# Kernel optimization log

Hardware: AMD Instinct MI355X
Metric: run time of the kernel (lower is better)

Reference implementation:

```python
import jax, jax.numpy as jnp
import numpy as np

EMBED_DICT = 200
EMBED_DIM = 16
HIDDEN = 32
LSTM_DIM = 256
B, C, L = 8192, 16, 64
END_IDX = 1  # stand-in for token_list.index('<End>')


def _lin(k, i, o):
    return jax.random.normal(k, (i, o), jnp.float32) * (1.0 / np.sqrt(i))


def setup_inputs() -> dict:
    key = jax.random.key(0)
    ks = jax.random.split(key, 20)
    feat_in = EMBED_DIM * 14 + LSTM_DIM  # 480
    z = lambda n: jnp.zeros((n,), jnp.float32)
    return {
        "trees": jax.random.randint(ks[0], (B, 1 + C, 17), 0, L),
        "lstm_out_list": jax.random.normal(ks[1], (B, L, 1, LSTM_DIM), jnp.float32),
        "first_notes": jax.random.normal(ks[2], (B, EMBED_DIM), jnp.float32),
        "train": 1,
        "embedding": jax.random.normal(ks[3], (EMBED_DICT, EMBED_DIM), jnp.float32) * 0.05,
        "leaf_end_W": _lin(ks[4], EMBED_DIM, HIDDEN), "leaf_end_b": z(HIDDEN),
        "lc_W1": _lin(ks[5], feat_in, HIDDEN * 4), "lc_b1": z(HIDDEN * 4),
        "lc_W2": _lin(ks[6], HIDDEN * 4, HIDDEN), "lc_b2": z(HIDDEN),
        "cs_W1": _lin(ks[7], HIDDEN * 2, HIDDEN * 4), "cs_b1": z(HIDDEN * 4),
        "cs_W2": _lin(ks[8], HIDDEN * 4, HIDDEN), "cs_b2": z(HIDDEN),
        "nf_W1": _lin(ks[9], feat_in, HIDDEN * 4), "nf_b1": z(HIDDEN * 4),
        "nf_W2": _lin(ks[10], HIDDEN * 4, HIDDEN), "nf_b2": z(HIDDEN),
        "cb_W1": _lin(ks[11], HIDDEN * 2, HIDDEN * 4), "cb_b1": z(HIDDEN * 4),
        "cb_W2": _lin(ks[12], HIDDEN * 4, HIDDEN), "cb_b2": z(HIDDEN),
        "ff_W1": _lin(ks[13], HIDDEN, HIDDEN), "ff_b1": z(HIDDEN),
        "ff_W2": _lin(ks[14], HIDDEN, HIDDEN), "ff_b2": z(HIDDEN),
        "ts_W": _lin(ks[15], HIDDEN, 1), "ts_b": z(1),
    }


def _mlp2(x, W1, b1, W2, b2):
    # Linear -> ReLU -> Linear -> ReLU (matches nn.Sequential blocks)
    return jax.nn.relu(jax.nn.relu(x @ W1 + b1) @ W2 + b2)


def reference(trees, lstm_out_list, first_notes, train, embedding,
              leaf_end_W, leaf_end_b, lc_W1, lc_b1, lc_W2, lc_b2,
              cs_W1, cs_b1, cs_W2, cs_b2, nf_W1, nf_b1, nf_W2, nf_b2,
              cb_W1, cb_b1, cb_W2, cb_b2, ff_W1, ff_b1, ff_W2, ff_b2,
              ts_W, ts_b):
    Bn = trees.shape[0]
    root = trees[:, 0, :]        # (B, 17)
    leaves = trees[:, 1:, :]     # (B, C, 17)
    Cn = leaves.shape[1]
    bidx = jnp.arange(Bn)

    # ---- leaf nodes: either leaf_end_ff(embed(type)) or leaf_child_ff(concat) ----
    leaf_tok = embedding[leaves[:, :, 2:-1]].reshape(Bn, Cn, -1)       # (B,C,224)
    leaf_ptr = lstm_out_list[bidx[:, None], leaves[:, :, -1], 0, :]    # (B,C,256)
    leaf_child = _mlp2(jnp.concatenate([leaf_tok, leaf_ptr], -1),
                       lc_W1, lc_b1, lc_W2, lc_b2)                     # (B,C,32)
    leaf_end = embedding[leaves[:, :, 2]] @ leaf_end_W + leaf_end_b    # (B,C,32)
    is_end = (leaves[:, :, 2] == END_IDX)[..., None]
    children = jnp.where(is_end, leaf_end, leaf_child)                 # (B,C,32)

    # ---- sequential left fold with child_sum_ff over children ----
    def step(carry, child):
        nxt = _mlp2(jnp.concatenate([carry, child], -1), cs_W1, cs_b1, cs_W2, cs_b2)
        return nxt, None
    child_summary, _ = jax.lax.scan(step, children[:, 0],
                                    jnp.moveaxis(children[:, 1:], 0, 1))  # (B,32)

    # ---- root node embedding + combine ----
    node_tok = embedding[root[:, 2:-1]].reshape(Bn, -1)                # (B,224)
    node_ptr = lstm_out_list[bidx, root[:, -1], 0, :]                  # (B,256)
    node_tmp = _mlp2(jnp.concatenate([node_tok, node_ptr], -1),
                     nf_W1, nf_b1, nf_W2, nf_b2)                       # (B,32)
    tree_sum = _mlp2(jnp.concatenate([node_tmp, child_summary], -1),
                     cb_W1, cb_b1, cb_W2, cb_b2)                       # (B,32)

    # ---- head: two linears (no activation) then score ----
    ff = (tree_sum @ ff_W1 + ff_b1) @ ff_W2 + ff_b2
    return ff @ ts_W + ts_b                                            # (B,1)
```

## Files before the change

### kernel.cpp

```cpp
#include <hip/hip_runtime.h>
#include <cstddef>


typedef __bf16 bf16x8 __attribute__((ext_vector_type(8)));
typedef __bf16 bf16x4 __attribute__((ext_vector_type(4)));
typedef float  f32x4  __attribute__((ext_vector_type(4)));

__global__ __launch_bounds__(256) void prep_kernel(
    const float* __restrict__ embedding,
    const float* __restrict__ leaf_end_W, const float* __restrict__ leaf_end_b,
    const float* __restrict__ lc_W1, const float* __restrict__ lc_W2,
    const float* __restrict__ nf_W1, const float* __restrict__ nf_W2,
    const float* __restrict__ cs_W1, const float* __restrict__ cs_W2,
    const float* __restrict__ cb_W1, const float* __restrict__ cb_W2,
    const float* __restrict__ ff_W1, const float* __restrict__ ff_b1,
    const float* __restrict__ ff_W2, const float* __restrict__ ff_b2,
    const float* __restrict__ ts_W, const float* __restrict__ ts_b,
    __bf16* __restrict__ lcW1T, __bf16* __restrict__ nfW1T,
    __bf16* __restrict__ lcW2T, __bf16* __restrict__ nfW2T,
    __bf16* __restrict__ emb_bf, float* __restrict__ endvec,
    __bf16* __restrict__ csW1Th, __bf16* __restrict__ csW1Tl,
    __bf16* __restrict__ cbW1Th, __bf16* __restrict__ cbW1Tl,
    __bf16* __restrict__ csW2Th, __bf16* __restrict__ csW2Tl,
    __bf16* __restrict__ cbW2Th, __bf16* __restrict__ cbW2Tl,
    float* __restrict__ vfin, float* __restrict__ cfin)
{
    const int id = blockIdx.x * 256 + threadIdx.x;
    if (id < 61440) {
        const int k = id >> 7, n = id & 127;
        lcW1T[n * 480 + k] = (__bf16)lc_W1[id];
    } else if (id < 122880) {
        const int e = id - 61440;
        const int k = e >> 7, n = e & 127;
        nfW1T[n * 480 + k] = (__bf16)nf_W1[e];
    } else if (id < 126976) {
        const int e = id - 122880;
        const int k = e >> 5, n = e & 31;
        lcW2T[n * 128 + k] = (__bf16)lc_W2[e];
    } else if (id < 131072) {
        const int e = id - 126976;
        const int k = e >> 5, n = e & 31;
        nfW2T[n * 128 + k] = (__bf16)nf_W2[e];
    } else if (id < 134272) {
        emb_bf[id - 131072] = (__bf16)embedding[id - 131072];
    } else if (id < 134304) {
        const int c = id - 134272;
        float a = leaf_end_b[c];
        #pragma unroll
        for (int d = 0; d < 16; ++d) a = fmaf(embedding[16 + d], leaf_end_W[d * 32 + c], a);
        endvec[c] = a;
    } else if (id < 142496) {
        const int e = id - 134304;
        const int k = e >> 7, n = e & 127;
        const float v = cs_W1[e];
        const __bf16 h = (__bf16)v;
        csW1Th[n * 64 + k] = h; csW1Tl[n * 64 + k] = (__bf16)(v - (float)h);
    } else if (id < 150688) {
        const int e = id - 142496;
        const int k = e >> 7, n = e & 127;
        const float v = cb_W1[e];
        const __bf16 h = (__bf16)v;
        cbW1Th[n * 64 + k] = h; cbW1Tl[n * 64 + k] = (__bf16)(v - (float)h);
    } else if (id < 154784) {
        const int e = id - 150688;
        const int k = e >> 5, n = e & 31;
        const float v = cs_W2[e];
        const __bf16 h = (__bf16)v;
        csW2Th[n * 128 + k] = h; csW2Tl[n * 128 + k] = (__bf16)(v - (float)h);
    } else if (id < 158880) {
        const int e = id - 154784;
        const int k = e >> 5, n = e & 31;
        const float v = cb_W2[e];
        const __bf16 h = (__bf16)v;
        cbW2Th[n * 128 + k] = h; cbW2Tl[n * 128 + k] = (__bf16)(v - (float)h);
    } else if (id < 158912) {
        const int c = id - 158880;
        float w2t[32];
        #pragma unroll
        for (int k = 0; k < 32; ++k) {
            float a = 0.f;
            for (int j = 0; j < 32; ++j) a = fmaf(ff_W2[k * 32 + j], ts_W[j], a);
            w2t[k] = a;
        }
        float a = 0.f;
        #pragma unroll
        for (int k = 0; k < 32; ++k) a = fmaf(ff_W1[c * 32 + k], w2t[k], a);
        vfin[c] = a;
    } else if (id == 158912) {
        float a = ts_b[0];
        for (int j = 0; j < 32; ++j) a = fmaf(ff_b2[j], ts_W[j], a);
        for (int k = 0; k < 32; ++k) {
            float w2t = 0.f;
            for (int j = 0; j < 32; ++j) w2t = fmaf(ff_W2[k * 32 + j], ts_W[j], w2t);
            a = fmaf(ff_b1[k], w2t, a);
        }
        cfin[0] = a;
    }
}

__global__ __launch_bounds__(256, 4) void mlp1_mfma(
    const int* __restrict__ trees,
    const float* __restrict__ lstm,
    const __bf16* __restrict__ lcW1T, const __bf16* __restrict__ nfW1T,
    const __bf16* __restrict__ lcW2T, const __bf16* __restrict__ nfW2T,
    const __bf16* __restrict__ emb_bf, const float* __restrict__ endvec,
    const float* __restrict__ lc_b1, const float* __restrict__ lc_b2,
    const float* __restrict__ nf_b1, const float* __restrict__ nf_b2,
    __bf16* __restrict__ childrenH, __bf16* __restrict__ childrenL,
    __bf16* __restrict__ node_tmpH, __bf16* __restrict__ node_tmpL)
{
    __shared__ __align__(16) __bf16 emb_s[200 * 24];
    __shared__ __align__(16) __bf16 Hs[64][136];
    __shared__ float b1s[128], b2s[32], evs[32];
    __shared__ int   endf[64];

    const int tid = threadIdx.x;
    const int blk = blockIdx.x;
    const bool leaf = (blk < 2048);

    const __bf16* __restrict__ W1T = leaf ? lcW1T : nfW1T;
    const __bf16* __restrict__ W2T = leaf ? lcW2T : nfW2T;
    const float*  __restrict__ b1p = leaf ? lc_b1 : nf_b1;
    const float*  __restrict__ b2p = leaf ? lc_b2 : nf_b2;

    const int l  = tid & 63;
    const int w  = tid >> 6;
    const int lm = l & 15;
    const int kb = l >> 4;
    const int wm = w >> 1;
    const int wn = w & 1;

    const int* tb[2];
    const float* lb[2];
    #pragma unroll
    for (int i = 0; i < 2; ++i) {
        const int r = wm * 32 + i * 16 + lm;
        int b, trow;
        if (leaf) { const int R = blk * 64 + r; b = R >> 4; trow = 1 + (R & 15); }
        else      { b = (blk - 2048) * 64 + r; trow = 0; }
        const int* t = trees + (b * 17 + trow) * 17;
        tb[i] = t;
        lb[i] = lstm + ((size_t)b * 64 + (size_t)t[16]) * 256;
    }

    for (int i = tid; i < 3200; i += 256) {
        const int row = i >> 4, col = i & 15;
        emb_s[row * 24 + col] = emb_bf[i];
    }
    if (tid < 128) b1s[tid] = b1p[tid];
    if (tid < 32)  { b2s[tid] = b2p[tid]; evs[tid] = leaf ? endvec[tid] : 0.f; }
    if (tid < 64) {
        if (leaf) {
            const int R = blk * 64 + tid;
            const int b = R >> 4, trow = 1 + (R & 15);
            endf[tid] = (trees[(b * 17 + trow) * 17 + 2] == 1);
        } else endf[tid] = 0;
    }

    f32x4 acc[2][4];
    #pragma unroll
    for (int i = 0; i < 2; ++i)
        #pragma unroll
        for (int j = 0; j < 4; ++j) acc[i][j] = (f32x4){0.f, 0.f, 0.f, 0.f};

    __syncthreads();

    #pragma unroll
    for (int c = 0; c < 15; ++c) {
        bf16x8 wfr[4];
        #pragma unroll
        for (int ct = 0; ct < 4; ++ct) {
            const int n = wn * 64 + ct * 16 + lm;
            wfr[ct] = *(const bf16x8*)(W1T + n * 480 + c * 32 + kb * 8);
        }
        bf16x8 bfr[2];
        if (c < 7) {
            #pragma unroll
            for (int i = 0; i < 2; ++i) {
                const int tok = tb[i][2 + 2 * c + (kb >> 1)];
                bfr[i] = *(const bf16x8*)(emb_s + tok * 24 + (kb & 1) * 8);
            }
        } else {
            #pragma unroll
            for (int i = 0; i < 2; ++i) {
                const float* p = lb[i] + (c - 7) * 32 + kb * 8;
                const float4 u = *(const float4*)p;
                const float4 v = *(const float4*)(p + 4);
                bf16x8 t;
                t[0] = (__bf16)u.x; t[1] = (__bf16)u.y; t[2] = (__bf16)u.z; t[3] = (__bf16)u.w;
                t[4] = (__bf16)v.x; t[5] = (__bf16)v.y; t[6] = (__bf16)v.z; t[7] = (__bf16)v.w;
                bfr[i] = t;
            }
        }
        #pragma unroll
        for (int i = 0; i < 2; ++i)
            #pragma unroll
            for (int ct = 0; ct < 4; ++ct)
                acc[i][ct] = __builtin_amdgcn_mfma_f32_16x16x32_bf16(wfr[ct], bfr[i], acc[i][ct], 0, 0, 0);
    }

    #pragma unroll
    for (int i = 0; i < 2; ++i)
        #pragma unroll
        for (int ct = 0; ct < 4; ++ct) {
            const int wcol = wn * 64 + ct * 16 + 4 * kb;
            bf16x4 pk;
            #pragma unroll
            for (int rg = 0; rg < 4; ++rg) {
                float v = acc[i][ct][rg] + b1s[wcol + rg];
                v = v > 0.f ? v : 0.f;
                pk[rg] = (__bf16)v;
            }
            *(bf16x4*)&Hs[wm * 32 + i * 16 + lm][wcol] = pk;
        }
    __syncthreads();

    const int jn = w & 1, rb2 = 2 * (w >> 1);
    f32x4 acc2[2];
    acc2[0] = (f32x4){0.f, 0.f, 0.f, 0.f};
    acc2[1] = (f32x4){0.f, 0.f, 0.f, 0.f};

    #pragma unroll
    for (int kc = 0; kc < 4; ++kc) {
        const bf16x8 wf = *(const bf16x8*)(W2T + (jn * 16 + lm) * 128 + kc * 32 + kb * 8);
        #pragma unroll
        for (int i = 0; i < 2; ++i) {
            const bf16x8 hf = *(const bf16x8*)(&Hs[(rb2 + i) * 16 + lm][kc * 32 + kb * 8]);
            acc2[i] = __builtin_amdgcn_mfma_f32_16x16x32_bf16(wf, hf, acc2[i], 0, 0, 0);
        }
    }

    #pragma unroll
    for (int i = 0; i < 2; ++i) {
        const int orow = (rb2 + i) * 16 + lm;
        const int ocol = jn * 16 + 4 * kb;
        const bool isend = leaf && endf[orow];
        bf16x4 ph, pl;
        #pragma unroll
        for (int rg = 0; rg < 4; ++rg) {
            float v = acc2[i][rg] + b2s[ocol + rg];
            v = v > 0.f ? v : 0.f;
            if (isend) v = evs[ocol + rg];
            const __bf16 h = (__bf16)v;
            ph[rg] = h;
            pl[rg] = (__bf16)(v - (float)h);
        }
        if (leaf) {
            const size_t R = (size_t)blk * 64 + orow;
            *(bf16x4*)&childrenH[R * 32 + ocol] = ph;
            *(bf16x4*)&childrenL[R * 32 + ocol] = pl;
        } else {
            const size_t R = (size_t)(blk - 2048) * 64 + orow;
            *(bf16x4*)&node_tmpH[R * 32 + ocol] = ph;
            *(bf16x4*)&node_tmpL[R * 32 + ocol] = pl;
        }
    }
}

__global__ __launch_bounds__(256) void scan_mfma(
    const __bf16* __restrict__ childrenH, const __bf16* __restrict__ childrenL,
    const __bf16* __restrict__ node_tmpH, const __bf16* __restrict__ node_tmpL,
    const __bf16* __restrict__ csW1Th, const __bf16* __restrict__ csW1Tl,
    const __bf16* __restrict__ csW2Th, const __bf16* __restrict__ csW2Tl,
    const __bf16* __restrict__ cbW1Th, const __bf16* __restrict__ cbW1Tl,
    const __bf16* __restrict__ cbW2Th, const __bf16* __restrict__ cbW2Tl,
    const float* __restrict__ cs_b1, const float* __restrict__ cs_b2,
    const float* __restrict__ cb_b1, const float* __restrict__ cb_b2,
    const float* __restrict__ vfin_g, const float* __restrict__ cfin_g,
    float* __restrict__ out)
{
    __shared__ __align__(16) __bf16 Xh[32][72], Xl[32][72];
    __shared__ __align__(16) __bf16 Hh[32][136], Hl[32][136];
    __shared__ float b1a[128], b1b[128], b2a[32], b2b[32], vfin[32];
    __shared__ float psum[2][32];
    __shared__ float cfin_s;

    const int tid = threadIdx.x;
    const int l = tid & 63, w = tid >> 6;
    const int lm = l & 15, kb = l >> 4;

    if (tid < 128)      { b1a[tid] = cs_b1[tid]; b1b[tid] = cb_b1[tid]; }
    else if (tid < 160) { b2a[tid - 128] = cs_b2[tid - 128]; b2b[tid - 128] = cb_b2[tid - 128]; }
    else if (tid < 192) { vfin[tid - 160] = vfin_g[tid - 160]; }
    else if (tid == 192) cfin_s = cfin_g[0];

    bf16x8 W1r[2][2][2];
    #pragma unroll
    for (int nt = 0; nt < 2; ++nt)
        #pragma unroll
        for (int kc = 0; kc < 2; ++kc) {
            const int n = w * 32 + nt * 16 + lm;
            W1r[nt][kc][0] = *(const bf16x8*)(csW1Th + n * 64 + kc * 32 + kb * 8);
            W1r[nt][kc][1] = *(const bf16x8*)(csW1Tl + n * 64 + kc * 32 + kb * 8);
        }
    bf16x8 W2r[4][2];
    {
        const int n2 = (w & 1) * 16 + lm;
        #pragma unroll
        for (int kc = 0; kc < 4; ++kc) {
            W2r[kc][0] = *(const bf16x8*)(csW2Th + n2 * 128 + kc * 32 + kb * 8);
            W2r[kc][1] = *(const bf16x8*)(csW2Tl + n2 * 128 + kc * 32 + kb * 8);
        }
    }

    const size_t base = (size_t)blockIdx.x * 32;
    const int tt = tid >> 3, c4 = (tid & 7) * 4;

    {
        const size_t o0 = ((base + tt) * 16 + 0) * 32 + c4;
        const size_t o1 = ((base + tt) * 16 + 1) * 32 + c4;
        *(bf16x4*)&Xh[tt][c4]      = *(const bf16x4*)(childrenH + o0);
        *(bf16x4*)&Xl[tt][c4]      = *(const bf16x4*)(childrenL + o0);
        *(bf16x4*)&Xh[tt][32 + c4] = *(const bf16x4*)(childrenH + o1);
        *(bf16x4*)&Xl[tt][32 + c4] = *(const bf16x4*)(childrenL + o1);
    }
    __syncthreads();

    #pragma unroll 1
    for (int it = 1; it <= 16; ++it) {
        const bool fin = (it == 16);
        if (fin) {
            #pragma unroll
            for (int nt = 0; nt < 2; ++nt)
                #pragma unroll
                for (int kc = 0; kc < 2; ++kc) {
                    const int n = w * 32 + nt * 16 + lm;
                    W1r[nt][kc][0] = *(const bf16x8*)(cbW1Th + n * 64 + kc * 32 + kb * 8);
                    W1r[nt][kc][1] = *(const bf16x8*)(cbW1Tl + n * 64 + kc * 32 + kb * 8);
                }
            const int n2 = (w & 1) * 16 + lm;
            #pragma unroll
            for (int kc = 0; kc < 4; ++kc) {
                W2r[kc][0] = *(const bf16x8*)(cbW2Th + n2 * 128 + kc * 32 + kb * 8);
                W2r[kc][1] = *(const bf16x8*)(cbW2Tl + n2 * 128 + kc * 32 + kb * 8);
            }
        }
        const float* __restrict__ b1c = fin ? b1b : b1a;
        const float* __restrict__ b2c = fin ? b2b : b2a;

        bf16x4 pfh, pfl;
        const int pfmode = (it < 15) ? 1 : (it == 15 ? 2 : 0);
        if (pfmode == 1) {
            const size_t o = ((base + tt) * 16 + (it + 1)) * 32 + c4;
            pfh = *(const bf16x4*)(childrenH + o);
            pfl = *(const bf16x4*)(childrenL + o);
        } else if (pfmode == 2) {
            const size_t o = (base + tt) * 32 + c4;
            pfh = *(const bf16x4*)(node_tmpH + o);
            pfl = *(const bf16x4*)(node_tmpL + o);
        }

        bf16x8 xh[2][2], xl[2][2];
        #pragma unroll
        for (int tn = 0; tn < 2; ++tn)
            #pragma unroll
            for (int kc = 0; kc < 2; ++kc) {
                xh[tn][kc] = *(const bf16x8*)&Xh[tn * 16 + lm][kc * 32 + kb * 8];
                xl[tn][kc] = *(const bf16x8*)&Xl[tn * 16 + lm][kc * 32 + kb * 8];
            }
        f32x4 a1[2][2];
        #pragma unroll
        for (int tn = 0; tn < 2; ++tn)
            #pragma unroll
            for (int nt = 0; nt < 2; ++nt) {
                a1[tn][nt] = (f32x4){0.f, 0.f, 0.f, 0.f};
                #pragma unroll
                for (int kc = 0; kc < 2; ++kc) {
                    a1[tn][nt] = __builtin_amdgcn_mfma_f32_16x16x32_bf16(W1r[nt][kc][0], xh[tn][kc], a1[tn][nt], 0, 0, 0);
                    a1[tn][nt] = __builtin_amdgcn_mfma_f32_16x16x32_bf16(W1r[nt][kc][0], xl[tn][kc], a1[tn][nt], 0, 0, 0);
                    a1[tn][nt] = __builtin_amdgcn_mfma_f32_16x16x32_bf16(W1r[nt][kc][1], xh[tn][kc], a1[tn][nt], 0, 0, 0);
                }
            }
        #pragma unroll
        for (int tn = 0; tn < 2; ++tn)
            #pragma unroll
            for (int nt = 0; nt < 2; ++nt) {
                const int wcol = w * 32 + nt * 16 + 4 * kb;
                bf16x4 ph, pl;
                #pragma unroll
                for (int rg = 0; rg < 4; ++rg) {
                    float v = a1[tn][nt][rg] + b1c[wcol + rg];
                    v = v > 0.f ? v : 0.f;
                    const __bf16 h = (__bf16)v;
                    ph[rg] = h;
                    pl[rg] = (__bf16)(v - (float)h);
                }
                *(bf16x4*)&Hh[tn * 16 + lm][wcol] = ph;
                *(bf16x4*)&Hl[tn * 16 + lm][wcol] = pl;
            }
        __syncthreads();

        const int mt = w >> 1, jn = w & 1;
        f32x4 a2 = (f32x4){0.f, 0.f, 0.f, 0.f};
        #pragma unroll
        for (int kc = 0; kc < 4; ++kc) {
            const bf16x8 hh = *(const bf16x8*)&Hh[mt * 16 + lm][kc * 32 + kb * 8];
            const bf16x8 hl = *(const bf16x8*)&Hl[mt * 16 + lm][kc * 32 + kb * 8];
            a2 = __builtin_amdgcn_mfma_f32_16x16x32_bf16(W2r[kc][0], hh, a2, 0, 0, 0);
            a2 = __builtin_amdgcn_mfma_f32_16x16x32_bf16(W2r[kc][0], hl, a2, 0, 0, 0);
            a2 = __builtin_amdgcn_mfma_f32_16x16x32_bf16(W2r[kc][1], hh, a2, 0, 0, 0);
        }

        if (!fin) {
            const int cb_ = (it == 15) ? 32 : 0;
            const int ocol = jn * 16 + 4 * kb;
            bf16x4 ph, pl;
            #pragma unroll
            for (int rg = 0; rg < 4; ++rg) {
                float v = a2[rg] + b2c[ocol + rg];
                v = v > 0.f ? v : 0.f;
                const __bf16 h = (__bf16)v;
                ph[rg] = h;
                pl[rg] = (__bf16)(v - (float)h);
            }
            *(bf16x4*)&Xh[mt * 16 + lm][cb_ + ocol] = ph;
            *(bf16x4*)&Xl[mt * 16 + lm][cb_ + ocol] = pl;
            if (pfmode) {
                const int dst = (pfmode == 2) ? 0 : 32;
                *(bf16x4*)&Xh[tt][dst + c4] = pfh;
                *(bf16x4*)&Xl[tt][dst + c4] = pfl;
            }
            __syncthreads();
        } else {
            const int ocol = jn * 16 + 4 * kb;
            float p = 0.f;
            #pragma unroll
            for (int rg = 0; rg < 4; ++rg) {
                float v = a2[rg] + b2c[ocol + rg];
                v = v > 0.f ? v : 0.f;
                p = fmaf(v, vfin[ocol + rg], p);
            }
            p += __shfl_xor(p, 16, 64);
            p += __shfl_xor(p, 32, 64);
            if (kb == 0) psum[jn][mt * 16 + lm] = p;
            __syncthreads();
            if (tid < 32) out[base + tid] = cfin_s + psum[0][tid] + psum[1][tid];
        }
    }
}

extern "C" void kernel_launch(void* const* d_in, const int* in_sizes, int n_in,
                              void* d_out, int out_size, void* d_ws, size_t ws_size,
                              hipStream_t stream) {
    const int*   trees      = (const int*)d_in[0];
    const float* lstm       = (const float*)d_in[1];
    const float* embedding  = (const float*)d_in[4];
    const float* leaf_end_W = (const float*)d_in[5];
    const float* leaf_end_b = (const float*)d_in[6];
    const float* lc_W1 = (const float*)d_in[7];
    const float* lc_b1 = (const float*)d_in[8];
    const float* lc_W2 = (const float*)d_in[9];
    const float* lc_b2 = (const float*)d_in[10];
    const float* cs_W1 = (const float*)d_in[11];
    const float* cs_b1 = (const float*)d_in[12];
    const float* cs_W2 = (const float*)d_in[13];
    const float* cs_b2 = (const float*)d_in[14];
    const float* nf_W1 = (const float*)d_in[15];
    const float* nf_b1 = (const float*)d_in[16];
    const float* nf_W2 = (const float*)d_in[17];
    const float* nf_b2 = (const float*)d_in[18];
    const float* cb_W1 = (const float*)d_in[19];
    const float* cb_b1 = (const float*)d_in[20];
    const float* cb_W2 = (const float*)d_in[21];
    const float* cb_b2 = (const float*)d_in[22];
    const float* ff_W1 = (const float*)d_in[23];
    const float* ff_b1 = (const float*)d_in[24];
    const float* ff_W2 = (const float*)d_in[25];
    const float* ff_b2 = (const float*)d_in[26];
    const float* ts_W  = (const float*)d_in[27];
    const float* ts_b  = (const float*)d_in[28];

    char* ws = (char*)d_ws;
    __bf16* childrenH = (__bf16*)ws;
    __bf16* childrenL = (__bf16*)(ws + 8388608);
    __bf16* node_tmpH = (__bf16*)(ws + 16777216);
    __bf16* node_tmpL = (__bf16*)(ws + 17301504);
    __bf16* lcW1T    = (__bf16*)(ws + 17825792);
    __bf16* nfW1T    = (__bf16*)(ws + 17948672);
    __bf16* lcW2T    = (__bf16*)(ws + 18071552);
    __bf16* nfW2T    = (__bf16*)(ws + 18079744);
    __bf16* emb_bf   = (__bf16*)(ws + 18087936);
    float*  endvec   = (float*)(ws + 18094336);
    __bf16* csW1Th   = (__bf16*)(ws + 18094464);
    __bf16* csW1Tl   = (__bf16*)(ws + 18110848);
    __bf16* cbW1Th   = (__bf16*)(ws + 18127232);
    __bf16* cbW1Tl   = (__bf16*)(ws + 18143616);
    __bf16* csW2Th   = (__bf16*)(ws + 18160000);
    __bf16* csW2Tl   = (__bf16*)(ws + 18168192);
    __bf16* cbW2Th   = (__bf16*)(ws + 18176384);
    __bf16* cbW2Tl   = (__bf16*)(ws + 18184576);
    float*  vfin     = (float*)(ws + 18192768);
    float*  cfin     = (float*)(ws + 18192896);
    float*  outp     = (float*)d_out;

    prep_kernel<<<dim3(621), dim3(256), 0, stream>>>(
        embedding, leaf_end_W, leaf_end_b, lc_W1, lc_W2, nf_W1, nf_W2,
        cs_W1, cs_W2, cb_W1, cb_W2, ff_W1, ff_b1, ff_W2, ff_b2, ts_W, ts_b,
        lcW1T, nfW1T, lcW2T, nfW2T, emb_bf, endvec,
        csW1Th, csW1Tl, cbW1Th, cbW1Tl, csW2Th, csW2Tl, cbW2Th, cbW2Tl,
        vfin, cfin);

    mlp1_mfma<<<dim3(2176), dim3(256), 0, stream>>>(
        trees, lstm, lcW1T, nfW1T, lcW2T, nfW2T, emb_bf, endvec,
        lc_b1, lc_b2, nf_b1, nf_b2, childrenH, childrenL, node_tmpH, node_tmpL);

    scan_mfma<<<dim3(256), dim3(256), 0, stream>>>(
        childrenH, childrenL, node_tmpH, node_tmpL,
        csW1Th, csW1Tl, csW2Th, csW2Tl, cbW1Th, cbW1Tl, cbW2Th, cbW2Tl,
        cs_b1, cs_b2, cb_b1, cb_b2, vfin, cfin, outp);
}
```

Before: 122.7 us.

## Stage W1 tiles through LDS in mlp1 and split scan work across 8 waves

In mlp1_mfma, each W1 k-chunk (128x32) is now loaded cooperatively once per block into shared memory, with a register prefetch of the next chunk. Each wave then reads its fragments from LDS instead of every wave fetching them from global memory, which cuts redundant global and L2 traffic. The cost is two extra barriers per k-chunk. Separately, scan_mfma moves to 512 threads: eight waves split the first MLP's rows (tn) and columns (q), while only four waves do the second MLP. The aim is more latency hiding in the serial scan, at the price of idle waves during the second MLP and extra barrier participants.

```diff
diff --git a/kernel.cpp b/kernel.cpp
--- a/kernel.cpp
+++ b/kernel.cpp
@@ -110,6 +110,7 @@
     __bf16* __restrict__ node_tmpH, __bf16* __restrict__ node_tmpL)
 {
     __shared__ __align__(16) __bf16 emb_s[200 * 24];
+    __shared__ __align__(16) __bf16 Ws[128 * 40];
     __shared__ __align__(16) __bf16 Hs[64][136];
     __shared__ float b1s[128], b2s[32], evs[32];
     __shared__ int   endf[64];
@@ -129,6 +130,10 @@
     const int kb = l >> 4;
     const int wm = w >> 1;
     const int wn = w & 1;
+
+    const int sn = tid & 127, sh = tid >> 7;
+    const __bf16* __restrict__ wsrc = W1T + sn * 480 + sh * 16;
+    const int wdst = sn * 40 + sh * 16;
 
     const int* tb[2];
     const float* lb[2];
@@ -163,15 +168,18 @@
         #pragma unroll
         for (int j = 0; j < 4; ++j) acc[i][j] = (f32x4){0.f, 0.f, 0.f, 0.f};
 
+    bf16x8 st0 = *(const bf16x8*)(wsrc);
+    bf16x8 st1 = *(const bf16x8*)(wsrc + 8);
+
     __syncthreads();
 
     #pragma unroll
     for (int c = 0; c < 15; ++c) {
-        bf16x8 wfr[4];
-        #pragma unroll
-        for (int ct = 0; ct < 4; ++ct) {
-            const int n = wn * 64 + ct * 16 + lm;
-            wfr[ct] = *(const bf16x8*)(W1T + n * 480 + c * 32 + kb * 8);
+        *(bf16x8*)&Ws[wdst]     = st0;
+        *(bf16x8*)&Ws[wdst + 8] = st1;
+        if (c < 14) {
+            st0 = *(const bf16x8*)(wsrc + (c + 1) * 32);
+            st1 = *(const bf16x8*)(wsrc + (c + 1) * 32 + 8);
         }
         bf16x8 bfr[2];
         if (c < 7) {
@@ -192,11 +200,19 @@
                 bfr[i] = t;
             }
         }
+        __syncthreads();
+        bf16x8 wfr[4];
+        #pragma unroll
+        for (int ct = 0; ct < 4; ++ct) {
+            const int n = wn * 64 + ct * 16 + lm;
+            wfr[ct] = *(const bf16x8*)&Ws[n * 40 + kb * 8];
+        }
         #pragma unroll
         for (int i = 0; i < 2; ++i)
             #pragma unroll
             for (int ct = 0; ct < 4; ++ct)
                 acc[i][ct] = __builtin_amdgcn_mfma_f32_16x16x32_bf16(wfr[ct], bfr[i], acc[i][ct], 0, 0, 0);
+        __syncthreads();
     }
 
     #pragma unroll
@@ -257,7 +273,7 @@
     }
 }
 
-__global__ __launch_bounds__(256) void scan_mfma(
+__global__ __launch_bounds__(512) void scan_mfma(
     const __bf16* __restrict__ childrenH, const __bf16* __restrict__ childrenL,
     const __bf16* __restrict__ node_tmpH, const __bf16* __restrict__ node_tmpL,
     const __bf16* __restrict__ csW1Th, const __bf16* __restrict__ csW1Tl,
@@ -278,6 +294,8 @@
     const int tid = threadIdx.x;
     const int l = tid & 63, w = tid >> 6;
     const int lm = l & 15, kb = l >> 4;
+    const int q  = w >> 1;
+    const int tn = w & 1;
 
     if (tid < 128)      { b1a[tid] = cs_b1[tid]; b1b[tid] = cb_b1[tid]; }
     else if (tid < 160) { b2a[tid - 128] = cs_b2[tid - 128]; b2b[tid - 128] = cb_b2[tid - 128]; }
@@ -289,12 +307,12 @@
     for (int nt = 0; nt < 2; ++nt)
         #pragma unroll
         for (int kc = 0; kc < 2; ++kc) {
-            const int n = w * 32 + nt * 16 + lm;
+            const int n = q * 32 + nt * 16 + lm;
             W1r[nt][kc][0] = *(const bf16x8*)(csW1Th + n * 64 + kc * 32 + kb * 8);
             W1r[nt][kc][1] = *(const bf16x8*)(csW1Tl + n * 64 + kc * 32 + kb * 8);
         }
     bf16x8 W2r[4][2];
-    {
+    if (w < 4) {
         const int n2 = (w & 1) * 16 + lm;
         #pragma unroll
         for (int kc = 0; kc < 4; ++kc) {
@@ -304,9 +322,9 @@
     }
 
     const size_t base = (size_t)blockIdx.x * 32;
-    const int tt = tid >> 3, c4 = (tid & 7) * 4;
-
-    {
+    const int tt = (tid & 255) >> 3, c4 = (tid & 7) * 4;
+
+    if (tid < 256) {
         const size_t o0 = ((base + tt) * 16 + 0) * 32 + c4;
         const size_t o1 = ((base + tt) * 16 + 1) * 32 + c4;
         *(bf16x4*)&Xh[tt][c4]      = *(const bf16x4*)(childrenH + o0);
@@ -324,15 +342,17 @@
             for (int nt = 0; nt < 2; ++nt)
                 #pragma unroll
                 for (int kc = 0; kc < 2; ++kc) {
-                    const int n = w * 32 + nt * 16 + lm;
+                    const int n = q * 32 + nt * 16 + lm;
                     W1r[nt][kc][0] = *(const bf16x8*)(cbW1Th + n * 64 + kc * 32 + kb * 8);
                     W1r[nt][kc][1] = *(const bf16x8*)(cbW1Tl + n * 64 + kc * 32 + kb * 8);
                 }
-            const int n2 = (w & 1) * 16 + lm;
-            #pragma unroll
-            for (int kc = 0; kc < 4; ++kc) {
-                W2r[kc][0] = *(const bf16x8*)(cbW2Th + n2 * 128 + kc * 32 + kb * 8);
-                W2r[kc][1] = *(const bf16x8*)(cbW2Tl + n2 * 128 + kc * 32 + kb * 8);
+            if (w < 4) {
+                const int n2 = (w & 1) * 16 + lm;
+                #pragma unroll
+                for (int kc = 0; kc < 4; ++kc) {
+                    W2r[kc][0] = *(const bf16x8*)(cbW2Th + n2 * 128 + kc * 32 + kb * 8);
+                    W2r[kc][1] = *(const bf16x8*)(cbW2Tl + n2 * 128 + kc * 32 + kb * 8);
+                }
             }
         }
         const float* __restrict__ b1c = fin ? b1b : b1a;
@@ -340,99 +360,101 @@
 
         bf16x4 pfh, pfl;
         const int pfmode = (it < 15) ? 1 : (it == 15 ? 2 : 0);
-        if (pfmode == 1) {
-            const size_t o = ((base + tt) * 16 + (it + 1)) * 32 + c4;
-            pfh = *(const bf16x4*)(childrenH + o);
-            pfl = *(const bf16x4*)(childrenL + o);
-        } else if (pfmode == 2) {
-            const size_t o = (base + tt) * 32 + c4;
-            pfh = *(const bf16x4*)(node_tmpH + o);
-            pfl = *(const bf16x4*)(node_tmpL + o);
-        }
-
-        bf16x8 xh[2][2], xl[2][2];
-        #pragma unroll
-        for (int tn = 0; tn < 2; ++tn)
+        if (tid < 256) {
+            if (pfmode == 1) {
+                const size_t o = ((base + tt) * 16 + (it + 1)) * 32 + c4;
+                pfh = *(const bf16x4*)(childrenH + o);
+                pfl = *(const bf16x4*)(childrenL + o);
+            } else if (pfmode == 2) {
+                const size_t o = (base + tt) * 32 + c4;
+                pfh = *(const bf16x4*)(node_tmpH + o);
+                pfl = *(const bf16x4*)(node_tmpL + o);
+            }
+        }
+
+        bf16x8 xh[2], xl[2];
+        #pragma unroll
+        for (int kc = 0; kc < 2; ++kc) {
+            xh[kc] = *(const bf16x8*)&Xh[tn * 16 + lm][kc * 32 + kb * 8];
+            xl[kc] = *(const bf16x8*)&Xl[tn * 16 + lm][kc * 32 + kb * 8];
+        }
+        f32x4 a1[2];
+        #pragma unroll
+        for (int nt = 0; nt < 2; ++nt) {
+            a1[nt] = (f32x4){0.f, 0.f, 0.f, 0.f};
             #pragma unroll
             for (int kc = 0; kc < 2; ++kc) {
-                xh[tn][kc] = *(const bf16x8*)&Xh[tn * 16 + lm][kc * 32 + kb * 8];
-                xl[tn][kc] = *(const bf16x8*)&Xl[tn * 16 + lm][kc * 32 + kb * 8];
-            }
-        f32x4 a1[2][2];
-        #pragma unroll
-        for (int tn = 0; tn < 2; ++tn)
-            #pragma unroll
-            for (int nt = 0; nt < 2; ++nt) {
-                a1[tn][nt] = (f32x4){0.f, 0.f, 0.f, 0.f};
-                #pragma unroll
-                for (int kc = 0; kc < 2; ++kc) {
-                    a1[tn][nt] = __builtin_amdgcn_mfma_f32_16x16x32_bf16(W1r[nt][kc][0], xh[tn][kc], a1[tn][nt], 0, 0, 0);
-                    a1[tn][nt] = __builtin_amdgcn_mfma_f32_16x16x32_bf16(W1r[nt][kc][0], xl[tn][kc], a1[tn][nt], 0, 0, 0);
-                    a1[tn][nt] = __builtin_amdgcn_mfma_f32_16x16x32_bf16(W1r[nt][kc][1], xh[tn][kc], a1[tn][nt], 0, 0, 0);
-                }
-            }
-        #pragma unroll
-        for (int tn = 0; tn < 2; ++tn)
-            #pragma unroll
-            for (int nt = 0; nt < 2; ++nt) {
-                const int wcol = w * 32 + nt * 16 + 4 * kb;
+                a1[nt] = __builtin_amdgcn_mfma_f32_16x16x32_bf16(W1r[nt][kc][0], xh[kc], a1[nt], 0, 0, 0);
+                a1[nt] = __builtin_amdgcn_mfma_f32_16x16x32_bf16(W1r[nt][kc][0], xl[kc], a1[nt], 0, 0, 0);
+                a1[nt] = __builtin_amdgcn_mfma_f32_16x16x32_bf16(W1r[nt][kc][1], xh[kc], a1[nt], 0, 0, 0);
+            }
+        }
+        #pragma unroll
+        for (int nt = 0; nt < 2; ++nt) {
+            const int wcol = q * 32 + nt * 16 + 4 * kb;
+            bf16x4 ph, pl;
+            #pragma unroll
+            for (int rg = 0; rg < 4; ++rg) {
+                float v = a1[nt][rg] + b1c[wcol + rg];
+                v = v > 0.f ? v : 0.f;
+                const __bf16 h = (__bf16)v;
+                ph[rg] = h;
+                pl[rg] = (__bf16)(v - (float)h);
+            }
+            *(bf16x4*)&Hh[tn * 16 + lm][wcol] = ph;
+            *(bf16x4*)&Hl[tn * 16 + lm][wcol] = pl;
+        }
+        __syncthreads();
+
+        f32x4 a2 = (f32x4){0.f, 0.f, 0.f, 0.f};
+        const int mt = w >> 1, jn = w & 1;
+        if (w < 4) {
+            #pragma unroll
+            for (int kc = 0; kc < 4; ++kc) {
+                const bf16x8 hh = *(const bf16x8*)&Hh[mt * 16 + lm][kc * 32 + kb * 8];
+                const bf16x8 hl = *(const bf16x8*)&Hl[mt * 16 + lm][kc * 32 + kb * 8];
+                a2 = __builtin_amdgcn_mfma_f32_16x16x32_bf16(W2r[kc][0], hh, a2, 0, 0, 0);
+                a2 = __builtin_amdgcn_mfma_f32_16x16x32_bf16(W2r[kc][0], hl, a2, 0, 0, 0);
+                a2 = __builtin_amdgcn_mfma_f32_16x16x32_bf16(W2r[kc][1], hh, a2, 0, 0, 0);
+            }
+        }
+
+        if (!fin) {
+            const int cb_ = (it == 15) ? 32 : 0;
+            if (w < 4) {
+                const int ocol = jn * 16 + 4 * kb;
                 bf16x4 ph, pl;
                 #pragma unroll
                 for (int rg = 0; rg < 4; ++rg) {
-                    float v = a1[tn][nt][rg] + b1c[wcol + rg];
+                    float v = a2[rg] + b2c[ocol + rg];
                     v = v > 0.f ? v : 0.f;
                     const __bf16 h = (__bf16)v;
                     ph[rg] = h;
                     pl[rg] = (__bf16)(v - (float)h);
                 }
-                *(bf16x4*)&Hh[tn * 16 + lm][wcol] = ph;
-                *(bf16x4*)&Hl[tn * 16 + lm][wcol] = pl;
-            }
-        __syncthreads();
-
-        const int mt = w >> 1, jn = w & 1;
-        f32x4 a2 = (f32x4){0.f, 0.f, 0.f, 0.f};
-        #pragma unroll
-        for (int kc = 0; kc < 4; ++kc) {
-            const bf16x8 hh = *(const bf16x8*)&Hh[mt * 16 + lm][kc * 32 + kb * 8];
-            const bf16x8 hl = *(const bf16x8*)&Hl[mt * 16 + lm][kc * 32 + kb * 8];
-            a2 = __builtin_amdgcn_mfma_f32_16x16x32_bf16(W2r[kc][0], hh, a2, 0, 0, 0);
-            a2 = __builtin_amdgcn_mfma_f32_16x16x32_bf16(W2r[kc][0], hl, a2, 0, 0, 0);
-            a2 = __builtin_amdgcn_mfma_f32_16x16x32_bf16(W2r[kc][1], hh, a2, 0, 0, 0);
-        }
-
-        if (!fin) {
-            const int cb_ = (it == 15) ? 32 : 0;
-            const int ocol = jn * 16 + 4 * kb;
-            bf16x4 ph, pl;
-            #pragma unroll
-            for (int rg = 0; rg < 4; ++rg) {
-                float v = a2[rg] + b2c[ocol + rg];
-                v = v > 0.f ? v : 0.f;
-                const __bf16 h = (__bf16)v;
-                ph[rg] = h;
-                pl[rg] = (__bf16)(v - (float)h);
-            }
-            *(bf16x4*)&Xh[mt * 16 + lm][cb_ + ocol] = ph;
-            *(bf16x4*)&Xl[mt * 16 + lm][cb_ + ocol] = pl;
-            if (pfmode) {
+                *(bf16x4*)&Xh[mt * 16 + lm][cb_ + ocol] = ph;
+                *(bf16x4*)&Xl[mt * 16 + lm][cb_ + ocol] = pl;
+            }
+            if (tid < 256 && pfmode) {
                 const int dst = (pfmode == 2) ? 0 : 32;
                 *(bf16x4*)&Xh[tt][dst + c4] = pfh;
                 *(bf16x4*)&Xl[tt][dst + c4] = pfl;
             }
             __syncthreads();
         } else {
-            const int ocol = jn * 16 + 4 * kb;
-            float p = 0.f;
-            #pragma unroll
-            for (int rg = 0; rg < 4; ++rg) {
-                float v = a2[rg] + b2c[ocol + rg];
-                v = v > 0.f ? v : 0.f;
-                p = fmaf(v, vfin[ocol + rg], p);
-            }
-            p += __shfl_xor(p, 16, 64);
-            p += __shfl_xor(p, 32, 64);
-            if (kb == 0) psum[jn][mt * 16 + lm] = p;
+            if (w < 4) {
+                const int ocol = jn * 16 + 4 * kb;
+                float p = 0.f;
+                #pragma unroll
+                for (int rg = 0; rg < 4; ++rg) {
+                    float v = a2[rg] + b2c[ocol + rg];
+                    v = v > 0.f ? v : 0.f;
+                    p = fmaf(v, vfin[ocol + rg], p);
+                }
+                p += __shfl_xor(p, 16, 64);
+                p += __shfl_xor(p, 32, 64);
+                if (kb == 0) psum[jn][mt * 16 + lm] = p;
+            }
             __syncthreads();
             if (tid < 32) out[base + tid] = cfin_s + psum[0][tid] + psum[1][tid];
         }
@@ -504,7 +526,7 @@
         trees, lstm, lcW1T, nfW1T, lcW2T, nfW2T, emb_bf, endvec,
         lc_b1, lc_b2, nf_b1, nf_b2, childrenH, childrenL, node_tmpH, node_tmpL);
 
-    scan_mfma<<<dim3(256), dim3(256), 0, stream>>>(
+    scan_mfma<<<dim3(256), dim3(512), 0, stream>>>(
         childrenH, childrenL, node_tmpH, node_tmpL,
         csW1Th, csW1Tl, csW2Th, csW2Tl, cbW1Th, cbW1Tl, cbW2Th, cbW2Tl,
         cs_b1, cs_b2, cb_b1, cb_b2, vfin, cfin, outp);
```

After: 126.0 us. +2.7%, slower.
